# Kernel tuning notes

Measured on AMD Instinct MI355X. Metric: run time of the kernel, lower is better.

## Reference

```python
import jax, jax.numpy as jnp
import numpy as np

N_NODES = 50000
N_EDGES = 800000
D_IN = 256
D_OUT = 256


def setup_inputs() -> dict:
    key = jax.random.key(0)
    k1, k2, k3, k4, k5 = jax.random.split(key, 5)
    x = jax.random.normal(k1, (N_NODES, D_IN), dtype=jnp.float32)
    edge_row = jax.random.randint(k2, (N_EDGES,), 0, N_NODES, dtype=jnp.int32)
    edge_col = jax.random.randint(k3, (N_EDGES,), 0, N_NODES, dtype=jnp.int32)
    edge_vals = jax.random.uniform(k4, (N_EDGES,), dtype=jnp.float32)
    weight = jax.random.normal(k5, (D_IN, D_OUT), dtype=jnp.float32)
    bias = jnp.zeros((D_OUT,), dtype=jnp.float32)
    return {"x": x, "edge_row": edge_row, "edge_col": edge_col,
            "edge_vals": edge_vals, "weight": weight, "bias": bias}


def reference(x, edge_row, edge_col, edge_vals, weight, bias):
    # training=False, dropout=0.0 -> dropout is a no-op.
    # Dense matmul: xw = x @ W   [N, D_out]
    xw = x @ weight
    # SpMM over COO adjacency: out[r] += vals[e] * xw[c] for edge e=(r,c)
    msgs = edge_vals[:, None] * xw[edge_col]            # [E, D_out]
    out = jax.ops.segment_sum(msgs, edge_row, num_segments=N_NODES)
    # bias + activation epilogue
    return jax.nn.relu(out + bias)
```

## Files before the change

kernel.cpp:

```cpp
#include <hip/hip_runtime.h>

#define N_NODES 50000
#define N_EDGES 800000
#define D 256

#define E4 (N_EDGES / 4)
#define BCAP 64

#define NSLICE 8
#define SLICE_ROWS (N_NODES / NSLICE)
#define SCB 2048
#define SC_WGS (SCB / NSLICE)
#define SC_CHUNK ((E4 + SC_WGS - 1) / SC_WGS)

#define XBLKS ((N_NODES * D / 4 + 255) / 256)
#define WBLKS (D * D / 256)
#define PGRID (SCB + XBLKS + WBLKS)

typedef __attribute__((ext_vector_type(8))) short short8;
typedef __attribute__((ext_vector_type(4))) float f32x4;

typedef const __attribute__((address_space(1))) unsigned int* as1_u32p;
typedef __attribute__((address_space(3))) unsigned int* as3_u32p;

__device__ __forceinline__ unsigned short f2bf(float f) {
    unsigned int u = __float_as_uint(f);
    u = (u + 0x7fffu + ((u >> 16) & 1u)) >> 16;
    return (unsigned short)u;
}

__global__ __launch_bounds__(256) void prep_kernel(const int4* __restrict__ erow4,
                                                   const int4* __restrict__ ecol4,
                                                   const float4* __restrict__ evals4,
                                                   const float4* __restrict__ x,
                                                   ushort4* __restrict__ xh,
                                                   const float* __restrict__ W,
                                                   unsigned short* __restrict__ Wt,
                                                   int* __restrict__ count,
                                                   int2* __restrict__ spay) {
    int b = blockIdx.x;
    if (b < SCB) {
        int sl   = b & (NSLICE - 1);
        int wi   = b >> 3;
        int lo   = sl * SLICE_ROWS;
        int hi   = lo + SLICE_ROWS;
        int base = wi * SC_CHUNK;
        int end  = base + SC_CHUNK;
        if (end > E4) end = E4;

        for (int i = base + (int)threadIdx.x; i < end; i += 256) {
            int4 r = erow4[i];
            bool m0 = (r.x >= lo) & (r.x < hi);
            bool m1 = (r.y >= lo) & (r.y < hi);
            bool m2 = (r.z >= lo) & (r.z < hi);
            bool m3 = (r.w >= lo) & (r.w < hi);
            if (m0 | m1 | m2 | m3) {
                int4   c = ecol4[i];
                float4 v = evals4[i];
                if (m0) { int p = atomicAdd(&count[r.x], 1); if (p < BCAP) spay[r.x * BCAP + p] = make_int2(c.x, __float_as_int(v.x)); }
                if (m1) { int p = atomicAdd(&count[r.y], 1); if (p < BCAP) spay[r.y * BCAP + p] = make_int2(c.y, __float_as_int(v.y)); }
                if (m2) { int p = atomicAdd(&count[r.z], 1); if (p < BCAP) spay[r.z * BCAP + p] = make_int2(c.z, __float_as_int(v.z)); }
                if (m3) { int p = atomicAdd(&count[r.w], 1); if (p < BCAP) spay[r.w * BCAP + p] = make_int2(c.w, __float_as_int(v.w)); }
            }
        }
    } else if (b < SCB + XBLKS) {
        int i = (b - SCB) * 256 + threadIdx.x;
        float4 v = x[i];
        xh[i] = make_ushort4(f2bf(v.x), f2bf(v.y), f2bf(v.z), f2bf(v.w));
    } else {
        int idx = (b - SCB - XBLKS) * 256 + threadIdx.x;
        int k = idx >> 8, n = idx & 255;
        Wt[n * 256 + k] = f2bf(W[idx]);
    }
}

__global__ __launch_bounds__(256) void aggregate_kernel(const unsigned short* __restrict__ xh,
                                                        const int* __restrict__ count,
                                                        const int2* __restrict__ spay,
                                                        unsigned short* __restrict__ aggh) {
    int gid  = blockIdx.x * 256 + threadIdx.x;
    int row  = gid >> 6;
    int lane = threadIdx.x & 63;
    if (row >= N_NODES) return;
    int s = row * BCAP;
    int c = count[row];
    if (c > BCAP) c = BCAP;
    int e = s + c;
    float a0 = 0.f, a1 = 0.f, a2 = 0.f, a3 = 0.f;
    int i = s;
    for (; i + 12 <= e; i += 12) {
        int2 p[12];
        uint2 q[12];
#pragma unroll
        for (int j = 0; j < 12; ++j) p[j] = spay[i + j];
#pragma unroll
        for (int j = 0; j < 12; ++j)
            q[j] = ((const uint2*)(xh + (size_t)p[j].x * D))[lane];
#pragma unroll
        for (int j = 0; j < 12; ++j) {
            float v = __int_as_float(p[j].y);
            a0 += v * __uint_as_float(q[j].x << 16);
            a1 += v * __uint_as_float(q[j].x & 0xffff0000u);
            a2 += v * __uint_as_float(q[j].y << 16);
            a3 += v * __uint_as_float(q[j].y & 0xffff0000u);
        }
    }
    for (; i + 4 <= e; i += 4) {
        int2 p[4];
        uint2 q[4];
#pragma unroll
        for (int j = 0; j < 4; ++j) p[j] = spay[i + j];
#pragma unroll
        for (int j = 0; j < 4; ++j)
            q[j] = ((const uint2*)(xh + (size_t)p[j].x * D))[lane];
#pragma unroll
        for (int j = 0; j < 4; ++j) {
            float v = __int_as_float(p[j].y);
            a0 += v * __uint_as_float(q[j].x << 16);
            a1 += v * __uint_as_float(q[j].x & 0xffff0000u);
            a2 += v * __uint_as_float(q[j].y << 16);
            a3 += v * __uint_as_float(q[j].y & 0xffff0000u);
        }
    }
    for (; i < e; ++i) {
        int2  p = spay[i];
        float v = __int_as_float(p.y);
        uint2 q = ((const uint2*)(xh + (size_t)p.x * D))[lane];
        a0 += v * __uint_as_float(q.x << 16);
        a1 += v * __uint_as_float(q.x & 0xffff0000u);
        a2 += v * __uint_as_float(q.y << 16);
        a3 += v * __uint_as_float(q.y & 0xffff0000u);
    }
    ushort4 o = make_ushort4(f2bf(a0), f2bf(a1), f2bf(a2), f2bf(a3));
    ((ushort4*)(aggh + (size_t)row * D))[lane] = o;
}

__global__ __launch_bounds__(256) void gemm_mfma(const unsigned short* __restrict__ A,
                                                 const unsigned short* __restrict__ Wt,
                                                 const float* __restrict__ bias,
                                                 float* __restrict__ out) {
    __shared__ unsigned short As[128 * 32];
    __shared__ unsigned short Bs[128 * 32];

    int t    = threadIdx.x;
    int w    = t >> 6;
    int lane = t & 63;
    int wm   = w & 1;
    int wn   = w >> 1;
    int mblk = blockIdx.x >> 1;
    int nblk = blockIdx.x & 1;
    int m0   = mblk * 128;
    int n0   = nblk * 128;

    f32x4 acc[4][4];
#pragma unroll
    for (int i = 0; i < 4; ++i)
#pragma unroll
        for (int j = 0; j < 4; ++j) acc[i][j] = (f32x4){0.f, 0.f, 0.f, 0.f};

    int lq = lane >> 2;
    int lr = lane & 3;

    for (int k0 = 0; k0 < D; k0 += 32) {
#pragma unroll
        for (int i = 0; i < 2; ++i) {
            int r0 = i * 64 + w * 16;
            int gm = m0 + r0 + lq;
            if (gm > N_NODES - 1) gm = N_NODES - 1;
            const unsigned short* gp = A + (size_t)gm * D + k0 + lr * 8;
            __builtin_amdgcn_global_load_lds((as1_u32p)gp, (as3_u32p)(As + r0 * 32), 16, 0, 0);
        }
#pragma unroll
        for (int i = 0; i < 2; ++i) {
            int r0 = i * 64 + w * 16;
            int gn = n0 + r0 + lq;
            const unsigned short* gp = Wt + (size_t)gn * D + k0 + lr * 8;
            __builtin_amdgcn_global_load_lds((as1_u32p)gp, (as3_u32p)(Bs + r0 * 32), 16, 0, 0);
        }
        __syncthreads();

        short8 af[4], bf[4];
        int kq = (lane >> 4) * 8;
        int lm = lane & 15;
#pragma unroll
        for (int mt = 0; mt < 4; ++mt)
            af[mt] = *(const short8*)(As + (wm * 64 + mt * 16 + lm) * 32 + kq);
#pragma unroll
        for (int nt = 0; nt < 4; ++nt)
            bf[nt] = *(const short8*)(Bs + (wn * 64 + nt * 16 + lm) * 32 + kq);
#pragma unroll
        for (int mt = 0; mt < 4; ++mt)
#pragma unroll
            for (int nt = 0; nt < 4; ++nt)
                acc[mt][nt] = __builtin_amdgcn_mfma_f32_16x16x32_bf16(af[mt], bf[nt], acc[mt][nt], 0, 0, 0);
        __syncthreads();
    }

    int cl = lane & 15;
    int cr = (lane >> 4) * 4;
#pragma unroll
    for (int nt = 0; nt < 4; ++nt) {
        int n = n0 + wn * 64 + nt * 16 + cl;
        float b = bias[n];
#pragma unroll
        for (int mt = 0; mt < 4; ++mt) {
            int mbase = m0 + wm * 64 + mt * 16 + cr;
#pragma unroll
            for (int r = 0; r < 4; ++r) {
                int m = mbase + r;
                if (m < N_NODES) {
                    float v = acc[mt][nt][r] + b;
                    out[(size_t)m * D + n] = v > 0.f ? v : 0.f;
                }
            }
        }
    }
}

extern "C" void kernel_launch(void* const* d_in, const int* in_sizes, int n_in,
                              void* d_out, int out_size, void* d_ws, size_t ws_size,
                              hipStream_t stream) {
    const float* x     = (const float*)d_in[0];
    const int*   erow  = (const int*)d_in[1];
    const int*   ecol  = (const int*)d_in[2];
    const float* evals = (const float*)d_in[3];
    const float* W     = (const float*)d_in[4];
    const float* bias  = (const float*)d_in[5];
    float*       out   = (float*)d_out;

    char* ws = (char*)d_ws;
    unsigned short* xh   = (unsigned short*)ws;  ws += (size_t)N_NODES * D * 2;
    unsigned short* aggh = (unsigned short*)ws;  ws += (size_t)N_NODES * D * 2;
    unsigned short* Wt   = (unsigned short*)ws;  ws += (size_t)D * D * 2;
    int* count           = (int*)ws;             ws += (size_t)N_NODES * sizeof(int);

    int2* spay = (int2*)out;

    hipMemsetAsync(count, 0, (size_t)N_NODES * sizeof(int), stream);

    prep_kernel<<<PGRID, 256, 0, stream>>>(
        (const int4*)erow, (const int4*)ecol, (const float4*)evals,
        (const float4*)x, (ushort4*)xh, W, Wt, count, spay);

    int ablocks = (N_NODES * 64 + 255) / 256;
    aggregate_kernel<<<ablocks, 256, 0, stream>>>(xh, count, spay, aggh);

    int gblocks = ((N_NODES + 127) / 128) * 2;
    gemm_mfma<<<gblocks, 256, 0, stream>>>(aggh, Wt, bias, out);
}
```

Before: 221.0 us.

## Split aggregation feature dimension across two blocks per row group

The aggregate kernel now assigns each wavefront half of a row's 256 features, with each lane loading 4 bytes instead of 8. Grid size doubles to 25000 blocks, and the block index is remapped so the two halves of a 4-row group are launched near each other. The aim is more parallelism and memory-level concurrency for the gathers. The cost is that the edge payload and count are read twice, and each gather issues narrower loads.

```diff
diff --git a/kernel.cpp b/kernel.cpp
--- a/kernel.cpp
+++ b/kernel.cpp
@@ -16,6 +16,8 @@
 #define XBLKS ((N_NODES * D / 4 + 255) / 256)
 #define WBLKS (D * D / 256)
 #define PGRID (SCB + XBLKS + WBLKS)
+
+#define AG_BLOCKS 25000
 
 typedef __attribute__((ext_vector_type(8))) short short8;
 typedef __attribute__((ext_vector_type(4))) float f32x4;
@@ -78,61 +80,58 @@
                                                         const int* __restrict__ count,
                                                         const int2* __restrict__ spay,
                                                         unsigned short* __restrict__ aggh) {
-    int gid  = blockIdx.x * 256 + threadIdx.x;
-    int row  = gid >> 6;
-    int lane = threadIdx.x & 63;
-    if (row >= N_NODES) return;
+    int b     = blockIdx.x;
+    int dhalf = (b >> 2) & 1;
+    int rblk  = (b >> 3) * 4 + (b & 3);
+    int row   = rblk * 4 + (threadIdx.x >> 6);
+    int lane  = threadIdx.x & 63;
+    const unsigned short* xbase = xh + dhalf * 128 + lane * 2;
+
     int s = row * BCAP;
     int c = count[row];
     if (c > BCAP) c = BCAP;
     int e = s + c;
-    float a0 = 0.f, a1 = 0.f, a2 = 0.f, a3 = 0.f;
+    float a0 = 0.f, a1 = 0.f;
     int i = s;
     for (; i + 12 <= e; i += 12) {
         int2 p[12];
-        uint2 q[12];
+        unsigned q[12];
 #pragma unroll
         for (int j = 0; j < 12; ++j) p[j] = spay[i + j];
 #pragma unroll
         for (int j = 0; j < 12; ++j)
-            q[j] = ((const uint2*)(xh + (size_t)p[j].x * D))[lane];
+            q[j] = *(const unsigned*)(xbase + (size_t)p[j].x * D);
 #pragma unroll
         for (int j = 0; j < 12; ++j) {
             float v = __int_as_float(p[j].y);
-            a0 += v * __uint_as_float(q[j].x << 16);
-            a1 += v * __uint_as_float(q[j].x & 0xffff0000u);
-            a2 += v * __uint_as_float(q[j].y << 16);
-            a3 += v * __uint_as_float(q[j].y & 0xffff0000u);
+            a0 += v * __uint_as_float(q[j] << 16);
+            a1 += v * __uint_as_float(q[j] & 0xffff0000u);
         }
     }
     for (; i + 4 <= e; i += 4) {
         int2 p[4];
-        uint2 q[4];
+        unsigned q[4];
 #pragma unroll
         for (int j = 0; j < 4; ++j) p[j] = spay[i + j];
 #pragma unroll
         for (int j = 0; j < 4; ++j)
-            q[j] = ((const uint2*)(xh + (size_t)p[j].x * D))[lane];
+            q[j] = *(const unsigned*)(xbase + (size_t)p[j].x * D);
 #pragma unroll
         for (int j = 0; j < 4; ++j) {
             float v = __int_as_float(p[j].y);
-            a0 += v * __uint_as_float(q[j].x << 16);
-            a1 += v * __uint_as_float(q[j].x & 0xffff0000u);
-            a2 += v * __uint_as_float(q[j].y << 16);
-            a3 += v * __uint_as_float(q[j].y & 0xffff0000u);
+            a0 += v * __uint_as_float(q[j] << 16);
+            a1 += v * __uint_as_float(q[j] & 0xffff0000u);
         }
     }
     for (; i < e; ++i) {
-        int2  p = spay[i];
+        int2 p = spay[i];
         float v = __int_as_float(p.y);
-        uint2 q = ((const uint2*)(xh + (size_t)p.x * D))[lane];
-        a0 += v * __uint_as_float(q.x << 16);
-        a1 += v * __uint_as_float(q.x & 0xffff0000u);
-        a2 += v * __uint_as_float(q.y << 16);
-        a3 += v * __uint_as_float(q.y & 0xffff0000u);
-    }
-    ushort4 o = make_ushort4(f2bf(a0), f2bf(a1), f2bf(a2), f2bf(a3));
-    ((ushort4*)(aggh + (size_t)row * D))[lane] = o;
+        unsigned q = *(const unsigned*)(xbase + (size_t)p.x * D);
+        a0 += v * __uint_as_float(q << 16);
+        a1 += v * __uint_as_float(q & 0xffff0000u);
+    }
+    unsigned o = (unsigned)f2bf(a0) | ((unsigned)f2bf(a1) << 16);
+    *(unsigned*)(aggh + (size_t)row * D + dhalf * 128 + lane * 2) = o;
 }
 
 __global__ __launch_bounds__(256) void gemm_mfma(const unsigned short* __restrict__ A,
@@ -242,8 +241,7 @@
         (const int4*)erow, (const int4*)ecol, (const float4*)evals,
         (const float4*)x, (ushort4*)xh, W, Wt, count, spay);
 
-    int ablocks = (N_NODES * 64 + 255) / 256;
-    aggregate_kernel<<<ablocks, 256, 0, stream>>>(xh, count, spay, aggh);
+    aggregate_kernel<<<AG_BLOCKS, 256, 0, stream>>>(xh, count, spay, aggh);
 
     int gblocks = ((N_NODES + 127) / 128) * 2;
     gemm_mfma<<<gblocks, 256, 0, stream>>>(aggh, Wt, bias, out);
```

Result: slower. 229.5 us (+3.9%).

## Fuse SpMM aggregation and MFMA GEMM into one kernel via swizzled LDS tile

Applied to the files above, without the earlier changes.

Merges the aggregation and GEMM kernels. Each 512-thread block gathers 64 aggregated rows in bf16 directly into an XOR-swizzled LDS tile, then multiplies that tile by the full 256-wide weight with MFMA. This removes the global round trip of the bf16 aggregate buffer and one launch. The bucket payload also moves from the output buffer into workspace. The trade-off is that each block now covers the full N dimension with a smaller M tile, re-streams W per block, and needs more LDS, which can lower occupancy.

```diff
diff --git a/kernel.cpp b/kernel.cpp
--- a/kernel.cpp
+++ b/kernel.cpp
@@ -16,6 +16,8 @@
 #define XBLKS ((N_NODES * D / 4 + 255) / 256)
 #define WBLKS (D * D / 256)
 #define PGRID (SCB + XBLKS + WBLKS)
+
+#define MT_BLOCKS ((N_NODES + 63) / 64)
 
 typedef __attribute__((ext_vector_type(8))) short short8;
 typedef __attribute__((ext_vector_type(4))) float f32x4;
@@ -74,122 +76,115 @@
     }
 }
 
-__global__ __launch_bounds__(256) void aggregate_kernel(const unsigned short* __restrict__ xh,
-                                                        const int* __restrict__ count,
-                                                        const int2* __restrict__ spay,
-                                                        unsigned short* __restrict__ aggh) {
-    int gid  = blockIdx.x * 256 + threadIdx.x;
-    int row  = gid >> 6;
-    int lane = threadIdx.x & 63;
-    if (row >= N_NODES) return;
-    int s = row * BCAP;
-    int c = count[row];
-    if (c > BCAP) c = BCAP;
-    int e = s + c;
-    float a0 = 0.f, a1 = 0.f, a2 = 0.f, a3 = 0.f;
-    int i = s;
-    for (; i + 12 <= e; i += 12) {
-        int2 p[12];
-        uint2 q[12];
-#pragma unroll
-        for (int j = 0; j < 12; ++j) p[j] = spay[i + j];
-#pragma unroll
-        for (int j = 0; j < 12; ++j)
-            q[j] = ((const uint2*)(xh + (size_t)p[j].x * D))[lane];
-#pragma unroll
-        for (int j = 0; j < 12; ++j) {
-            float v = __int_as_float(p[j].y);
-            a0 += v * __uint_as_float(q[j].x << 16);
-            a1 += v * __uint_as_float(q[j].x & 0xffff0000u);
-            a2 += v * __uint_as_float(q[j].y << 16);
-            a3 += v * __uint_as_float(q[j].y & 0xffff0000u);
-        }
-    }
-    for (; i + 4 <= e; i += 4) {
-        int2 p[4];
-        uint2 q[4];
-#pragma unroll
-        for (int j = 0; j < 4; ++j) p[j] = spay[i + j];
-#pragma unroll
-        for (int j = 0; j < 4; ++j)
-            q[j] = ((const uint2*)(xh + (size_t)p[j].x * D))[lane];
-#pragma unroll
-        for (int j = 0; j < 4; ++j) {
-            float v = __int_as_float(p[j].y);
-            a0 += v * __uint_as_float(q[j].x << 16);
-            a1 += v * __uint_as_float(q[j].x & 0xffff0000u);
-            a2 += v * __uint_as_float(q[j].y << 16);
-            a3 += v * __uint_as_float(q[j].y & 0xffff0000u);
-        }
-    }
-    for (; i < e; ++i) {
-        int2  p = spay[i];
-        float v = __int_as_float(p.y);
-        uint2 q = ((const uint2*)(xh + (size_t)p.x * D))[lane];
-        a0 += v * __uint_as_float(q.x << 16);
-        a1 += v * __uint_as_float(q.x & 0xffff0000u);
-        a2 += v * __uint_as_float(q.y << 16);
-        a3 += v * __uint_as_float(q.y & 0xffff0000u);
-    }
-    ushort4 o = make_ushort4(f2bf(a0), f2bf(a1), f2bf(a2), f2bf(a3));
-    ((ushort4*)(aggh + (size_t)row * D))[lane] = o;
-}
-
-__global__ __launch_bounds__(256) void gemm_mfma(const unsigned short* __restrict__ A,
-                                                 const unsigned short* __restrict__ Wt,
-                                                 const float* __restrict__ bias,
-                                                 float* __restrict__ out) {
-    __shared__ unsigned short As[128 * 32];
-    __shared__ unsigned short Bs[128 * 32];
-
-    int t    = threadIdx.x;
-    int w    = t >> 6;
-    int lane = t & 63;
-    int wm   = w & 1;
-    int wn   = w >> 1;
-    int mblk = blockIdx.x >> 1;
-    int nblk = blockIdx.x & 1;
-    int m0   = mblk * 128;
-    int n0   = nblk * 128;
-
-    f32x4 acc[4][4];
-#pragma unroll
-    for (int i = 0; i < 4; ++i)
+__global__ __launch_bounds__(512, 6) void agg_gemm(const unsigned short* __restrict__ xh,
+                                                   const int* __restrict__ count,
+                                                   const int2* __restrict__ spay,
+                                                   const unsigned short* __restrict__ Wt,
+                                                   const float* __restrict__ bias,
+                                                   float* __restrict__ out) {
+    __shared__ unsigned short As[64 * 256];
+    __shared__ unsigned short Bs[256 * 32];
+
+    int tid  = threadIdx.x;
+    int wid  = tid >> 6;
+    int lane = tid & 63;
+    int m0   = blockIdx.x * 64;
+
+#pragma unroll 1
+    for (int j = 0; j < 8; ++j) {
+        int rl  = wid * 8 + j;
+        int row = m0 + rl;
+        float a0 = 0.f, a1 = 0.f, a2 = 0.f, a3 = 0.f;
+        if (row < N_NODES) {
+            int s = row * BCAP;
+            int c = count[row];
+            if (c > BCAP) c = BCAP;
+            int e = s + c;
+            int i = s;
+            for (; i + 12 <= e; i += 12) {
+                int2 p[12];
+                uint2 q[12];
+#pragma unroll
+                for (int t = 0; t < 12; ++t) p[t] = spay[i + t];
+#pragma unroll
+                for (int t = 0; t < 12; ++t)
+                    q[t] = ((const uint2*)(xh + (size_t)p[t].x * D))[lane];
+#pragma unroll
+                for (int t = 0; t < 12; ++t) {
+                    float v = __int_as_float(p[t].y);
+                    a0 += v * __uint_as_float(q[t].x << 16);
+                    a1 += v * __uint_as_float(q[t].x & 0xffff0000u);
+                    a2 += v * __uint_as_float(q[t].y << 16);
+                    a3 += v * __uint_as_float(q[t].y & 0xffff0000u);
+                }
+            }
+            for (; i + 4 <= e; i += 4) {
+                int2 p[4];
+                uint2 q[4];
+#pragma unroll
+                for (int t = 0; t < 4; ++t) p[t] = spay[i + t];
+#pragma unroll
+                for (int t = 0; t < 4; ++t)
+                    q[t] = ((const uint2*)(xh + (size_t)p[t].x * D))[lane];
+#pragma unroll
+                for (int t = 0; t < 4; ++t) {
+                    float v = __int_as_float(p[t].y);
+                    a0 += v * __uint_as_float(q[t].x << 16);
+                    a1 += v * __uint_as_float(q[t].x & 0xffff0000u);
+                    a2 += v * __uint_as_float(q[t].y << 16);
+                    a3 += v * __uint_as_float(q[t].y & 0xffff0000u);
+                }
+            }
+            for (; i < e; ++i) {
+                int2  p = spay[i];
+                float v = __int_as_float(p.y);
+                uint2 q = ((const uint2*)(xh + (size_t)p.x * D))[lane];
+                a0 += v * __uint_as_float(q.x << 16);
+                a1 += v * __uint_as_float(q.x & 0xffff0000u);
+                a2 += v * __uint_as_float(q.y << 16);
+                a3 += v * __uint_as_float(q.y & 0xffff0000u);
+            }
+        }
+        ushort4 o = make_ushort4(f2bf(a0), f2bf(a1), f2bf(a2), f2bf(a3));
+        unsigned bw = (unsigned)rl * 512u + (((unsigned)lane * 8u) ^ (((unsigned)rl & 7u) << 4));
+        *(ushort4*)((char*)As + bw) = o;
+    }
+    __syncthreads();
+
+    int wm = wid & 1;
+    int wn = wid >> 1;
+    f32x4 acc[2][4];
+#pragma unroll
+    for (int i = 0; i < 2; ++i)
 #pragma unroll
         for (int j = 0; j < 4; ++j) acc[i][j] = (f32x4){0.f, 0.f, 0.f, 0.f};
 
-    int lq = lane >> 2;
-    int lr = lane & 3;
+    int kq = (lane >> 4) * 8;
+    int lm = lane & 15;
 
     for (int k0 = 0; k0 < D; k0 += 32) {
 #pragma unroll
-        for (int i = 0; i < 2; ++i) {
-            int r0 = i * 64 + w * 16;
-            int gm = m0 + r0 + lq;
-            if (gm > N_NODES - 1) gm = N_NODES - 1;
-            const unsigned short* gp = A + (size_t)gm * D + k0 + lr * 8;
-            __builtin_amdgcn_global_load_lds((as1_u32p)gp, (as3_u32p)(As + r0 * 32), 16, 0, 0);
-        }
-#pragma unroll
-        for (int i = 0; i < 2; ++i) {
-            int r0 = i * 64 + w * 16;
-            int gn = n0 + r0 + lq;
-            const unsigned short* gp = Wt + (size_t)gn * D + k0 + lr * 8;
-            __builtin_amdgcn_global_load_lds((as1_u32p)gp, (as3_u32p)(Bs + r0 * 32), 16, 0, 0);
+        for (int it = 0; it < 2; ++it) {
+            int idx  = it * 512 + tid;
+            int n    = idx >> 2;
+            int koff = (idx & 3) * 8;
+            const unsigned short* gp = Wt + (size_t)n * D + k0 + koff;
+            __builtin_amdgcn_global_load_lds((as1_u32p)gp, (as3_u32p)(Bs + n * 32 + koff), 16, 0, 0);
         }
         __syncthreads();
 
-        short8 af[4], bf[4];
-        int kq = (lane >> 4) * 8;
-        int lm = lane & 15;
-#pragma unroll
-        for (int mt = 0; mt < 4; ++mt)
-            af[mt] = *(const short8*)(As + (wm * 64 + mt * 16 + lm) * 32 + kq);
+        short8 af[2], bf[4];
+#pragma unroll
+        for (int mt = 0; mt < 2; ++mt) {
+            unsigned rl = (unsigned)(wm * 32 + mt * 16 + lm);
+            unsigned br = rl * 512u + ((((unsigned)(k0 + kq)) * 2u) ^ ((rl & 7u) << 4));
+            af[mt] = *(const short8*)((const char*)As + br);
+        }
 #pragma unroll
         for (int nt = 0; nt < 4; ++nt)
             bf[nt] = *(const short8*)(Bs + (wn * 64 + nt * 16 + lm) * 32 + kq);
 #pragma unroll
-        for (int mt = 0; mt < 4; ++mt)
+        for (int mt = 0; mt < 2; ++mt)
 #pragma unroll
             for (int nt = 0; nt < 4; ++nt)
                 acc[mt][nt] = __builtin_amdgcn_mfma_f32_16x16x32_bf16(af[mt], bf[nt], acc[mt][nt], 0, 0, 0);
@@ -200,11 +195,11 @@
     int cr = (lane >> 4) * 4;
 #pragma unroll
     for (int nt = 0; nt < 4; ++nt) {
-        int n = n0 + wn * 64 + nt * 16 + cl;
+        int n = wn * 64 + nt * 16 + cl;
         float b = bias[n];
 #pragma unroll
-        for (int mt = 0; mt < 4; ++mt) {
-            int mbase = m0 + wm * 64 + mt * 16 + cr;
+        for (int mt = 0; mt < 2; ++mt) {
+            int mbase = m0 + wm * 32 + mt * 16 + cr;
 #pragma unroll
             for (int r = 0; r < 4; ++r) {
                 int m = mbase + r;
@@ -229,12 +224,10 @@
     float*       out   = (float*)d_out;
 
     char* ws = (char*)d_ws;
-    unsigned short* xh   = (unsigned short*)ws;  ws += (size_t)N_NODES * D * 2;
-    unsigned short* aggh = (unsigned short*)ws;  ws += (size_t)N_NODES * D * 2;
-    unsigned short* Wt   = (unsigned short*)ws;  ws += (size_t)D * D * 2;
-    int* count           = (int*)ws;             ws += (size_t)N_NODES * sizeof(int);
-
-    int2* spay = (int2*)out;
+    unsigned short* xh = (unsigned short*)ws;  ws += (size_t)N_NODES * D * 2;
+    int2* spay         = (int2*)ws;            ws += (size_t)N_NODES * BCAP * 8;
+    unsigned short* Wt = (unsigned short*)ws;  ws += (size_t)D * D * 2;
+    int* count         = (int*)ws;             ws += (size_t)N_NODES * sizeof(int);
 
     hipMemsetAsync(count, 0, (size_t)N_NODES * sizeof(int), stream);
 
@@ -242,9 +235,5 @@
         (const int4*)erow, (const int4*)ecol, (const float4*)evals,
         (const float4*)x, (ushort4*)xh, W, Wt, count, spay);
 
-    int ablocks = (N_NODES * 64 + 255) / 256;
-    aggregate_kernel<<<ablocks, 256, 0, stream>>>(xh, count, spay, aggh);
-
-    int gblocks = ((N_NODES + 127) / 128) * 2;
-    gemm_mfma<<<gblocks, 256, 0, stream>>>(aggh, Wt, bias, out);
-}
+    agg_gemm<<<MT_BLOCKS, 512, 0, stream>>>(xh, count, spay, Wt, bias, out);
+}
```

Result: slower. 240.1 us (+8.7%).
